# Kernel tuning notes

Hardware: AMD Instinct MI355X
Metric: run time of the kernel (lower is better)

The kernel has to match this reference:

```python
import jax, jax.numpy as jnp
import numpy as np

B, S, D, H, L, V = 2, 512, 1024, 16, 12, 50257
HD = D // H
DFF = 4 * D


def _ln(x, g, b, eps=1e-5):
    m = jnp.mean(x, axis=-1, keepdims=True)
    v = jnp.var(x, axis=-1, keepdims=True)
    return (x - m) * jax.lax.rsqrt(v + eps) * g + b


def setup_inputs() -> dict:
    key = jax.random.key(0)
    ks = jax.random.split(key, 32)
    sc = 0.02
    n = lambda k, shape: (jax.random.normal(k, shape, dtype=jnp.float32) * sc)
    inp = {
        "input_ids": jax.random.randint(ks[0], (B, S), 0, V, dtype=jnp.int64),
        "attention_mask": jnp.ones((B, S), dtype=jnp.float32),
        "image_hidden_states": jax.random.normal(ks[1], (B, D), dtype=jnp.float32),
        # token embedding table (also used for position embeds and tied lm_head, as in source)
        "wte": n(ks[2], (V, D)),
        # feature_space_transformation_nn: Linear(1024,1024) -> ReLU -> Linear(1024,1024)
        "ft_W1": n(ks[3], (D, D)), "ft_b1": jnp.zeros((D,), jnp.float32),
        "ft_W2": n(ks[4], (D, D)), "ft_b2": jnp.zeros((D,), jnp.float32),
        # per-layer params, stacked on leading L dim
        "ln1_g": jnp.ones((L, D), jnp.float32), "ln1_b": jnp.zeros((L, D), jnp.float32),
        "Wattn": n(ks[5], (L, D, 3 * D)), "battn": jnp.zeros((L, 3 * D), jnp.float32),
        "Wuk": n(ks[6], (L, D, D)), "buk": jnp.zeros((L, D), jnp.float32),
        "Wuv": n(ks[7], (L, D, D)), "buv": jnp.zeros((L, D), jnp.float32),
        "Wproj": n(ks[8], (L, D, D)), "bproj": jnp.zeros((L, D), jnp.float32),
        "ln2_g": jnp.ones((L, D), jnp.float32), "ln2_b": jnp.zeros((L, D), jnp.float32),
        "Wfc": n(ks[9], (L, D, DFF)), "bfc": jnp.zeros((L, DFF), jnp.float32),
        "Wfc2": n(ks[10], (L, DFF, D)), "bfc2": jnp.zeros((L, D), jnp.float32),
        "lnf_g": jnp.ones((D,), jnp.float32), "lnf_b": jnp.zeros((D,), jnp.float32),
    }
    return inp


def _forward(input_ids, attention_mask, image_hidden_states, wte,
             ft_W1, ft_b1, ft_W2, ft_b2,
             ln1_g, ln1_b, Wattn, battn, Wuk, buk, Wuv, buv, Wproj, bproj,
             ln2_g, ln2_b, Wfc, bfc, Wfc2, bfc2, lnf_g, lnf_b):
    # image feature transformation: Linear -> ReLU -> Linear
    img = jax.nn.relu(image_hidden_states @ ft_W1 + ft_b1) @ ft_W2 + ft_b2  # [B,D]

    # NOTE: source uses wte (not wpe) for position embeddings — faithful reproduction
    h = wte[input_ids] + wte[jnp.arange(S)][None]  # [B,S,D]

    # extended attention mask with a prepended zero column for the image token
    mask_ext = (1.0 - attention_mask)[:, None, None, :] * -10000.0  # [B,1,1,S]
    mask_ext = jnp.concatenate([jnp.zeros((B, 1, 1, 1), mask_ext.dtype), mask_ext], axis=-1)  # [B,1,1,S+1]

    # causal mask over kv_len=S+1: query i sees keys j <= i+1 (image token always visible)
    causal = jnp.arange(S + 1)[None, :] <= (jnp.arange(S)[:, None] + 1)  # [S,S+1]

    def block(h, p):
        (l1g, l1b, Wa, ba, Wk, bk, Wv, bv, Wp, bp, l2g, l2b, Wf, bf, Wf2, bf2) = p
        x = _ln(h, l1g, l1b)
        qkv = x @ Wa + ba
        q, k, v = jnp.split(qkv, 3, axis=-1)  # each [B,S,D]
        ki = (img @ Wk + bk)[:, None, :]  # [B,1,D]
        vi = (img @ Wv + bv)[:, None, :]
        k = jnp.concatenate([ki, k], axis=1)  # [B,S+1,D]
        v = jnp.concatenate([vi, v], axis=1)
        sh = lambda t, n: t.reshape(B, n, H, HD).transpose(0, 2, 1, 3)
        qh, kh, vh = sh(q, S), sh(k, S + 1), sh(v, S + 1)
        s = jnp.einsum('bhqd,bhkd->bhqk', qh, kh) / jnp.sqrt(jnp.float32(HD))
        s = jnp.where(causal[None, None], s, jnp.float32(-10000.0))
        s = s + mask_ext
        a = jax.nn.softmax(s, axis=-1)
        o = jnp.einsum('bhqk,bhkd->bhqd', a, vh).transpose(0, 2, 1, 3).reshape(B, S, D)
        h = h + (o @ Wp + bp)
        x = _ln(h, l2g, l2b)
        h = h + (jax.nn.gelu(x @ Wf + bf, approximate=True) @ Wf2 + bf2)
        return h, None

    params = (ln1_g, ln1_b, Wattn, battn, Wuk, buk, Wuv, buv, Wproj, bproj,
              ln2_g, ln2_b, Wfc, bfc, Wfc2, bfc2)
    h, _ = jax.lax.scan(block, h, params)
    h = _ln(h, lnf_g, lnf_b)
    return h @ wte.T  # tied lm head -> [B,S,V]


def reference(input_ids, attention_mask, image_hidden_states, wte,
              ft_W1, ft_b1, ft_W2, ft_b2,
              ln1_g, ln1_b, Wattn, battn, Wuk, buk, Wuv, buv, Wproj, bproj,
              ln2_g, ln2_b, Wfc, bfc, Wfc2, bfc2, lnf_g, lnf_b):
    return _forward(input_ids, attention_mask, image_hidden_states, wte,
                    ft_W1, ft_b1, ft_W2, ft_b2,
                    ln1_g, ln1_b, Wattn, battn, Wuk, buk, Wuv, buv, Wproj, bproj,
                    ln2_g, ln2_b, Wfc, bfc, Wfc2, bfc2, lnf_g, lnf_b)
```

## Files before the change

kernel.cpp:

```cpp
#include <hip/hip_runtime.h>
#include <cstdint>


typedef __bf16 bf16x8 __attribute__((ext_vector_type(8)));
typedef __bf16 bf16x4 __attribute__((ext_vector_type(4)));
typedef float  f32x4  __attribute__((ext_vector_type(4)));

#define GLDS16(g, l) __builtin_amdgcn_global_load_lds( \
    (const __attribute__((address_space(1))) unsigned int*)(g), \
    (__attribute__((address_space(3))) unsigned int*)(l), 16, 0, 0)

#define SCHED_FENCE() __builtin_amdgcn_sched_barrier(0)

__device__ __forceinline__ float gelu_f(float x) {
    float u = 1.5957691216057308f * (x + 0.044715f * x * x * x);
    float e = __expf(u);
    float t = 1.0f - 2.0f / (e + 1.0f);
    return 0.5f * x * (1.0f + t);
}

__device__ __forceinline__ int fragoff(int row, int kh, int hi) {
    return row * 64 + ((kh * 32 + hi * 8) ^ ((row & 7) << 3));
}
__device__ __forceinline__ int fragoff32(int row, int hi) {
    return row * 32 + ((hi ^ ((row >> 1) & 3)) << 3);
}

__device__ __forceinline__ void tcvt_body(
    int id, const float* __restrict__ Wa, const float* __restrict__ Wp,
    const float* __restrict__ Wf, const float* __restrict__ Wf2,
    __bf16* __restrict__ oa, __bf16* __restrict__ op,
    __bf16* __restrict__ of, __bf16* __restrict__ of2, float* tile)
{
    const float* src; __bf16* dst; int K, N, kb, nb;
    if (id < 768)       { src = Wa;  dst = oa;  K = 1024; N = 3072; kb = id & 15; nb = id >> 4; }
    else if (id < 1024) { id -= 768;  src = Wp;  dst = op;  K = 1024; N = 1024; kb = id & 15; nb = id >> 4; }
    else if (id < 2048) { id -= 1024; src = Wf;  dst = of;  K = 1024; N = 4096; kb = id & 15; nb = id >> 4; }
    else                { id -= 2048; src = Wf2; dst = of2; K = 4096; N = 1024; kb = id & 63; nb = id >> 6; }
    const int k0 = kb * 64, n0 = nb * 64;
    const int t = threadIdx.x;
    #pragma unroll
    for (int i = 0; i < 4; i++) {
        int r = i * 16 + (t >> 4), c = (t & 15) * 4;
        float4 v = *reinterpret_cast<const float4*>(src + (long)(k0 + r) * N + n0 + c);
        tile[r * 65 + c] = v.x; tile[r * 65 + c + 1] = v.y;
        tile[r * 65 + c + 2] = v.z; tile[r * 65 + c + 3] = v.w;
    }
    __syncthreads();
    const int nrow = t >> 2, kc = (t & 3) * 16;
    bf16x8 o0, o1;
    #pragma unroll
    for (int i = 0; i < 8; i++) {
        o0[i] = (__bf16)tile[(kc + i) * 65 + nrow];
        o1[i] = (__bf16)tile[(kc + 8 + i) * 65 + nrow];
    }
    *reinterpret_cast<bf16x8*>(dst + (long)(n0 + nrow) * K + k0 + kc)     = o0;
    *reinterpret_cast<bf16x8*>(dst + (long)(n0 + nrow) * K + k0 + kc + 8) = o1;
}

__device__ __forceinline__ void wcvt_body(
    int id, const float* __restrict__ wte, __bf16* __restrict__ out, long nvalid)
{
    long base = (long)id * 8192 + threadIdx.x * 8;
    #pragma unroll
    for (int i = 0; i < 4; i++) {
        long e = base + (long)i * 2048;
        bf16x8 o;
        if (e < nvalid) {
            float4 a = *reinterpret_cast<const float4*>(wte + e);
            float4 b = *reinterpret_cast<const float4*>(wte + e + 4);
            o[0] = (__bf16)a.x; o[1] = (__bf16)a.y; o[2] = (__bf16)a.z; o[3] = (__bf16)a.w;
            o[4] = (__bf16)b.x; o[5] = (__bf16)b.y; o[6] = (__bf16)b.z; o[7] = (__bf16)b.w;
        } else {
            #pragma unroll
            for (int q = 0; q < 8; q++) o[q] = (__bf16)0.f;
        }
        *reinterpret_cast<bf16x8*>(out + e) = o;
    }
}

__global__ __launch_bounds__(256) void tcvt_std(
    const float* __restrict__ Wa, const float* __restrict__ Wp,
    const float* __restrict__ Wf, const float* __restrict__ Wf2,
    __bf16* __restrict__ oa, __bf16* __restrict__ op,
    __bf16* __restrict__ of, __bf16* __restrict__ of2)
{
    __shared__ float tile[64 * 65];
    tcvt_body(blockIdx.x, Wa, Wp, Wf, Wf2, oa, op, of, of2, tile);
}

__global__ __launch_bounds__(256) void wcvt_std(
    const float* __restrict__ wte, __bf16* __restrict__ out, long nvalid)
{
    wcvt_body(blockIdx.x, wte, out, nvalid);
}

__global__ __launch_bounds__(256) void gemv_part(
    const float* __restrict__ x, int xld,
    const float* __restrict__ W, long wzs,
    float* __restrict__ part, int K, int N)
{
    int jb = blockIdx.x, kz = blockIdx.y, z = blockIdx.z;
    int t = threadIdx.x;
    int j = (jb << 6) + (t & 63);
    int g = t >> 6;
    int klen = K / (gridDim.y * 4);
    int kbase = (kz * 4 + g) * klen;
    const float* Wp = W + (long)z * wzs + (long)kbase * N + j;
    const float* x0 = x + kbase;
    const float* x1 = x + xld + kbase;
    float a0 = 0.f, a1 = 0.f;
    for (int k = 0; k < klen; k++) {
        float wv = Wp[(long)k * N];
        a0 += x0[k] * wv;
        a1 += x1[k] * wv;
    }
    __shared__ float r0[4][64], r1[4][64];
    r0[g][t & 63] = a0; r1[g][t & 63] = a1;
    __syncthreads();
    if (t < 64) {
        a0 = r0[0][t] + r0[1][t] + r0[2][t] + r0[3][t];
        a1 = r1[0][t] + r1[1][t] + r1[2][t] + r1[3][t];
        long base = (long)(z * gridDim.y + kz) * 2 * N + (jb << 6) + t;
        part[base]     = a0;
        part[base + N] = a1;
    }
}

__global__ __launch_bounds__(256) void gemv_reduce(
    const float* __restrict__ part, const float* __restrict__ bias, long bzs,
    float* __restrict__ out, int N, int nz, int act)
{
    int idx = blockIdx.x * 256 + threadIdx.x;
    if (idx >= nz * 2 * N) return;
    int j  = idx % N;
    int bz = idx / N;
    int z  = bz >> 1;
    float s = bias[(long)z * bzs + j];
    const float* p = part + ((long)z * 8 * 2 + (bz & 1)) * N + j;
    #pragma unroll
    for (int kz = 0; kz < 8; kz++) s += p[(long)kz * 2 * N];
    if (act) s = fmaxf(s, 0.f);
    out[idx] = s;
}

__global__ __launch_bounds__(256) void gemv_kv_part(
    const float* __restrict__ img,
    const float* __restrict__ Wuk, const float* __restrict__ Wuv,
    float* __restrict__ part)
{
    int jb = blockIdx.x, kz = blockIdx.y, z = blockIdx.z;
    int t = threadIdx.x;
    int j = (jb << 6) + (t & 63);
    int g = t >> 6;
    int kbase = (kz * 4 + g) * 64;
    const float* W = (z < 12) ? (Wuk + (long)z * 1048576) : (Wuv + (long)(z - 12) * 1048576);
    const float* Wp = W + (long)kbase * 1024 + j;
    const float* x0 = img + kbase;
    const float* x1 = img + 1024 + kbase;
    float a0 = 0.f, a1 = 0.f;
    for (int k = 0; k < 64; k++) {
        float wv = Wp[(long)k * 1024];
        a0 += x0[k] * wv;
        a1 += x1[k] * wv;
    }
    __shared__ float r0[4][64], r1[4][64];
    r0[g][t & 63] = a0; r1[g][t & 63] = a1;
    __syncthreads();
    if (t < 64) {
        a0 = r0[0][t] + r0[1][t] + r0[2][t] + r0[3][t];
        a1 = r1[0][t] + r1[1][t] + r1[2][t] + r1[3][t];
        long base = (long)(z * 4 + kz) * 2 * 1024 + (jb << 6) + t;
        part[base]        = a0;
        part[base + 1024] = a1;
    }
}

__global__ __launch_bounds__(256) void gemv_kv_reduce(
    const float* __restrict__ part,
    const float* __restrict__ buk, const float* __restrict__ buv,
    float* __restrict__ imgk, float* __restrict__ imgv)
{
    int idx = blockIdx.x * 256 + threadIdx.x;
    int z = idx >> 11;
    int bsel = (idx >> 10) & 1;
    int j = idx & 1023;
    float s = (z < 12) ? buk[z * 1024 + j] : buv[(z - 12) * 1024 + j];
    const float* p = part + ((long)z * 4 * 2 + bsel) * 1024 + j;
    #pragma unroll
    for (int kz = 0; kz < 4; kz++) s += p[(long)kz * 2 * 1024];
    if (z < 12) imgk[z * 2048 + bsel * 1024 + j] = s;
    else        imgv[(z - 12) * 2048 + bsel * 1024 + j] = s;
}

__global__ __launch_bounds__(256) void embed_ln(
    const int* __restrict__ ids, const float* __restrict__ wte,
    float* __restrict__ h, __bf16* __restrict__ xb,
    const float* __restrict__ g, const float* __restrict__ b)
{
    int row = blockIdx.x;
    int s = row & 511;
    int t = threadIdx.x;
    long id = ids[row];
    float4 v1 = reinterpret_cast<const float4*>(wte + id * 1024)[t];
    float4 v2 = reinterpret_cast<const float4*>(wte + (long)s * 1024)[t];
    float4 v; v.x = v1.x + v2.x; v.y = v1.y + v2.y; v.z = v1.z + v2.z; v.w = v1.w + v2.w;
    reinterpret_cast<float4*>(h + (long)row * 1024)[t] = v;

    float s1 = v.x + v.y + v.z + v.w;
    float s2 = v.x * v.x + v.y * v.y + v.z * v.z + v.w * v.w;
    #pragma unroll
    for (int o = 32; o >= 1; o >>= 1) { s1 += __shfl_xor(s1, o); s2 += __shfl_xor(s2, o); }
    __shared__ float r1[4], r2[4];
    int w = t >> 6;
    if ((t & 63) == 0) { r1[w] = s1; r2[w] = s2; }
    __syncthreads();
    s1 = r1[0] + r1[1] + r1[2] + r1[3];
    s2 = r2[0] + r2[1] + r2[2] + r2[3];
    float mean = s1 * (1.0f / 1024.0f);
    float var  = s2 * (1.0f / 1024.0f) - mean * mean;
    float rstd = rsqrtf(var + 1e-5f);
    float4 gg = reinterpret_cast<const float4*>(g)[t];
    float4 bb = reinterpret_cast<const float4*>(b)[t];
    bf16x4 o;
    o[0] = (__bf16)((v.x - mean) * rstd * gg.x + bb.x);
    o[1] = (__bf16)((v.y - mean) * rstd * gg.y + bb.y);
    o[2] = (__bf16)((v.z - mean) * rstd * gg.z + bb.z);
    o[3] = (__bf16)((v.w - mean) * rstd * gg.w + bb.w);
    *reinterpret_cast<bf16x4*>(xb + (long)row * 1024 + t * 4) = o;
}

__global__ __launch_bounds__(256) void ln_k(
    const float* __restrict__ in, __bf16* __restrict__ out,
    const float* __restrict__ g, const float* __restrict__ b)
{
    int row = blockIdx.x, t = threadIdx.x;
    float4 v = reinterpret_cast<const float4*>(in + (long)row * 1024)[t];
    float s1 = v.x + v.y + v.z + v.w;
    float s2 = v.x * v.x + v.y * v.y + v.z * v.z + v.w * v.w;
    #pragma unroll
    for (int o = 32; o >= 1; o >>= 1) { s1 += __shfl_xor(s1, o); s2 += __shfl_xor(s2, o); }
    __shared__ float r1[4], r2[4];
    int w = t >> 6;
    if ((t & 63) == 0) { r1[w] = s1; r2[w] = s2; }
    __syncthreads();
    s1 = r1[0] + r1[1] + r1[2] + r1[3];
    s2 = r2[0] + r2[1] + r2[2] + r2[3];
    float mean = s1 * (1.0f / 1024.0f);
    float var  = s2 * (1.0f / 1024.0f) - mean * mean;
    float rstd = rsqrtf(var + 1e-5f);
    float4 gg = reinterpret_cast<const float4*>(g)[t];
    float4 bb = reinterpret_cast<const float4*>(b)[t];
    bf16x4 o;
    o[0] = (__bf16)((v.x - mean) * rstd * gg.x + bb.x);
    o[1] = (__bf16)((v.y - mean) * rstd * gg.y + bb.y);
    o[2] = (__bf16)((v.z - mean) * rstd * gg.z + bb.z);
    o[3] = (__bf16)((v.w - mean) * rstd * gg.w + bb.w);
    *reinterpret_cast<bf16x4*>(out + (long)row * 1024 + t * 4) = o;
}

template<int NP>
__global__ __launch_bounds__(256) void lnadd_k(
    float* __restrict__ h, const float* __restrict__ part,
    const float* __restrict__ bias,
    const float* __restrict__ g, const float* __restrict__ b,
    __bf16* __restrict__ out)
{
    int row = blockIdx.x, t = threadIdx.x;
    long off = (long)row * 1024 + t * 4;
    float4 v = *reinterpret_cast<const float4*>(h + off);
    #pragma unroll
    for (int sp = 0; sp < NP; sp++) {
        float4 pv = *reinterpret_cast<const float4*>(part + sp * 1048576L + off);
        v.x += pv.x; v.y += pv.y; v.z += pv.z; v.w += pv.w;
    }
    float4 bi = reinterpret_cast<const float4*>(bias)[t];
    v.x += bi.x; v.y += bi.y; v.z += bi.z; v.w += bi.w;
    *reinterpret_cast<float4*>(h + off) = v;

    float s1 = v.x + v.y + v.z + v.w;
    float s2 = v.x * v.x + v.y * v.y + v.z * v.z + v.w * v.w;
    #pragma unroll
    for (int o = 32; o >= 1; o >>= 1) { s1 += __shfl_xor(s1, o); s2 += __shfl_xor(s2, o); }
    __shared__ float r1[4], r2[4];
    int w = t >> 6;
    if ((t & 63) == 0) { r1[w] = s1; r2[w] = s2; }
    __syncthreads();
    s1 = r1[0] + r1[1] + r1[2] + r1[3];
    s2 = r2[0] + r2[1] + r2[2] + r2[3];
    float mean = s1 * (1.0f / 1024.0f);
    float var  = s2 * (1.0f / 1024.0f) - mean * mean;
    float rstd = rsqrtf(var + 1e-5f);
    float4 gg = reinterpret_cast<const float4*>(g)[t];
    float4 bb = reinterpret_cast<const float4*>(b)[t];
    bf16x4 o;
    o[0] = (__bf16)((v.x - mean) * rstd * gg.x + bb.x);
    o[1] = (__bf16)((v.y - mean) * rstd * gg.y + bb.y);
    o[2] = (__bf16)((v.z - mean) * rstd * gg.z + bb.z);
    o[3] = (__bf16)((v.w - mean) * rstd * gg.w + bb.w);
    *reinterpret_cast<bf16x4*>(out + off) = o;
}

__global__ __launch_bounds__(512, 4) void gemm_lm2(
    const __bf16* __restrict__ A, const __bf16* __restrict__ Bt,
    float* __restrict__ C, int N, int K, int GM, int GN)
{
    const int total = GM * GN;
    const int q = total >> 3, r = total & 7;
    const int x = blockIdx.x & 7, jj = blockIdx.x >> 3;
    const int w0 = (x < r) ? x * (q + 1) + jj : r * (q + 1) + (x - r) * q + jj;
    const int m0 = (w0 % GM) * 128;
    const int n0 = (w0 / GM) * 256;

    __shared__ __bf16 As[3][128 * 32];
    __shared__ __bf16 Bs[3][256 * 32];
    const int t = threadIdx.x;
    const int wid = t >> 6, lane = t & 63;
    const int lo = lane & 15, hi = lane >> 4;
    const int wr = wid >> 2, wc = wid & 3;

    f32x4 acc[4][4] = {};

    const int srow = t >> 2;
    const int skx  = (((t & 3) ^ ((srow >> 1) & 3)) << 3);
    const int sldst = t * 8;
    #define STLM(bf, kk) do { \
        GLDS16(A + (long)(m0 + srow) * K + (kk) + skx, &As[bf][sldst]); \
        GLDS16(Bt + (long)(n0 + srow)       * K + (kk) + skx, &Bs[bf][sldst]); \
        GLDS16(Bt + (long)(n0 + 128 + srow) * K + (kk) + skx, &Bs[bf][4096 + sldst]); \
    } while (0)

    const int T = K >> 5;
    STLM(0, 0);
    if (T > 1) STLM(1, 32);
    int bcur = 0;
    for (int it = 0; it < T; it++) {
        if (it + 2 < T) {
            int bst = bcur >= 1 ? bcur - 1 : bcur + 2;
            STLM(bst, (it + 2) * 32);
            asm volatile("s_waitcnt vmcnt(6)" ::: "memory");
        } else if (it + 1 < T) {
            asm volatile("s_waitcnt vmcnt(3)" ::: "memory");
        } else {
            asm volatile("s_waitcnt vmcnt(0)" ::: "memory");
        }
        SCHED_FENCE();
        __builtin_amdgcn_s_barrier();
        SCHED_FENCE();

        bf16x8 afr[4], bfr[4];
        #pragma unroll
        for (int mi = 0; mi < 4; mi++)
            afr[mi] = *reinterpret_cast<const bf16x8*>(&As[bcur][fragoff32(wr * 64 + mi * 16 + lo, hi)]);
        #pragma unroll
        for (int ni = 0; ni < 4; ni++)
            bfr[ni] = *reinterpret_cast<const bf16x8*>(&Bs[bcur][fragoff32(wc * 64 + ni * 16 + lo, hi)]);
        __builtin_amdgcn_s_setprio(1);
        #pragma unroll
        for (int mi = 0; mi < 4; mi++)
            #pragma unroll
            for (int ni = 0; ni < 4; ni++)
                acc[mi][ni] = __builtin_amdgcn_mfma_f32_16x16x32_bf16(afr[mi], bfr[ni], acc[mi][ni], 0, 0, 0);
        __builtin_amdgcn_s_setprio(0);

        SCHED_FENCE();
        __builtin_amdgcn_s_barrier();
        SCHED_FENCE();
        bcur = bcur < 2 ? bcur + 1 : 0;
    }
    #undef STLM

    #pragma unroll
    for (int mi = 0; mi < 4; mi++)
        #pragma unroll
        for (int ni = 0; ni < 4; ni++) {
            int col = n0 + wc * 64 + ni * 16 + lo;
            if (col >= N) continue;
            #pragma unroll
            for (int rr = 0; rr < 4; rr++) {
                int row = m0 + wr * 64 + mi * 16 + hi * 4 + rr;
                C[(long)row * N + col] = acc[mi][ni][rr];
            }
        }
}

template<int BN, int OUTBF16, int ACT, int PARTIAL>
__global__ __launch_bounds__(256) void gemm64(
    const __bf16* __restrict__ A, const __bf16* __restrict__ Bt,
    const float* __restrict__ bias, void* __restrict__ C,
    int N, int K, int GM, int GN, int NS)
{
    constexpr int NB = BN / 32;
    constexpr int LP = 2 + NB;
    const int total = GM * GN * NS;
    const int q = total >> 3, r = total & 7;
    const int x = blockIdx.x & 7, jj = blockIdx.x >> 3;
    const int w0 = (x < r) ? x * (q + 1) + jj : r * (q + 1) + (x - r) * q + jj;
    const int sp = w0 / (GM * GN);
    const int rem = w0 - sp * (GM * GN);
    const int m0 = (rem % GM) * 64;
    const int n0 = (rem / GM) * BN;

    __shared__ __bf16 As[3][64 * 64];
    __shared__ __bf16 Bs[3][BN * 64];
    const int t = threadIdx.x;
    const int wv = t >> 6, lane = t & 63;
    const int lo = lane & 15, hi = lane >> 4;
    const int wr = wv >> 1, wc = wv & 1;

    f32x4 acc[2][NB] = {};

    const int srow = t >> 3;
    const int skx  = (((t & 7) ^ (srow & 7)) << 3);
    const int sldst = t * 8;
    #define ST64(bf, kk) do { \
        _Pragma("unroll") \
        for (int i = 0; i < 2; i++) \
            GLDS16(A + (long)(m0 + i * 32 + srow) * K + (kk) + skx, &As[bf][i * 2048 + sldst]); \
        _Pragma("unroll") \
        for (int i = 0; i < NB; i++) \
            GLDS16(Bt + (long)(n0 + i * 32 + srow) * K + (kk) + skx, &Bs[bf][i * 2048 + sldst]); \
    } while (0)

    const int Ksp = K / NS;
    const int kbeg = sp * Ksp;
    const int T = Ksp >> 6;

    ST64(0, kbeg);
    if (T > 1) ST64(1, kbeg + 64);
    int bcur = 0;
    for (int it = 0; it < T; it++) {
        if (it + 2 < T) {
            int bst = bcur >= 1 ? bcur - 1 : bcur + 2;
            ST64(bst, kbeg + (it + 2) * 64);
            asm volatile("s_waitcnt vmcnt(%0)" :: "i"(2 * LP) : "memory");
        } else if (it + 1 < T) {
            asm volatile("s_waitcnt vmcnt(%0)" :: "i"(LP) : "memory");
        } else {
            asm volatile("s_waitcnt vmcnt(0)" ::: "memory");
        }
        SCHED_FENCE();
        __builtin_amdgcn_s_barrier();
        SCHED_FENCE();

        #pragma unroll
        for (int kh = 0; kh < 2; kh++) {
            bf16x8 afr[2], bfr[NB];
            #pragma unroll
            for (int mi = 0; mi < 2; mi++)
                afr[mi] = *reinterpret_cast<const bf16x8*>(&As[bcur][fragoff(wr * 32 + mi * 16 + lo, kh, hi)]);
            #pragma unroll
            for (int ni = 0; ni < NB; ni++)
                bfr[ni] = *reinterpret_cast<const bf16x8*>(&Bs[bcur][fragoff(wc * (BN / 2) + ni * 16 + lo, kh, hi)]);
            __builtin_amdgcn_s_setprio(1);
            #pragma unroll
            for (int mi = 0; mi < 2; mi++)
                #pragma unroll
                for (int ni = 0; ni < NB; ni++)
                    acc[mi][ni] = __builtin_amdgcn_mfma_f32_16x16x32_bf16(afr[mi], bfr[ni], acc[mi][ni], 0, 0, 0);
            __builtin_amdgcn_s_setprio(0);
        }

        SCHED_FENCE();
        __builtin_amdgcn_s_barrier();
        SCHED_FENCE();
        bcur = bcur < 2 ? bcur + 1 : 0;
    }
    #undef ST64

    const long coff = PARTIAL ? (long)sp * GM * 64 * N : 0;
    #pragma unroll
    for (int mi = 0; mi < 2; mi++)
        #pragma unroll
        for (int ni = 0; ni < NB; ni++) {
            int col = n0 + wc * (BN / 2) + ni * 16 + lo;
            float bv = (!PARTIAL && bias) ? bias[col] : 0.f;
            #pragma unroll
            for (int rr = 0; rr < 4; rr++) {
                int row = m0 + wr * 32 + mi * 16 + hi * 4 + rr;
                float v = acc[mi][ni][rr] + bv;
                if (ACT) v = gelu_f(v);
                if (OUTBF16) ((__bf16*)C)[(long)row * N + col] = (__bf16)v;
                else         ((float*)C)[coff + (long)row * N + col] = v;
            }
        }
}

template<int OUTBF16, int ACT, int RES>
__global__ __launch_bounds__(256) void gemm_bb(
    const __bf16* __restrict__ A, const __bf16* __restrict__ Bt,
    const float* __restrict__ bias, const float* __restrict__ res,
    void* __restrict__ C, int N, int K)
{
    __shared__ __bf16 As[64 * 32];
    __shared__ __bf16 Bs[64 * 32];
    const int t = threadIdx.x;
    const int m0 = blockIdx.x * 64;
    const int n0 = blockIdx.y * 64;
    const int w = t >> 6, lane = t & 63;
    const int lo = lane & 15, hi = lane >> 4;
    const int wr = w >> 1, wc = w & 1;

    f32x4 acc[2][2] = {};

    for (int k0 = 0; k0 < K; k0 += 32) {
        __syncthreads();
        GLDS16(A  + (long)(m0 + (t >> 2)) * K + k0 + ((t & 3) << 3), &As[t * 8]);
        GLDS16(Bt + (long)(n0 + (t >> 2)) * K + k0 + ((t & 3) << 3), &Bs[t * 8]);
        __syncthreads();
        bf16x8 afr[2], bfr[2];
        #pragma unroll
        for (int mi = 0; mi < 2; mi++)
            afr[mi] = *reinterpret_cast<const bf16x8*>(&As[(wr * 32 + mi * 16 + lo) * 32 + hi * 8]);
        #pragma unroll
        for (int ni = 0; ni < 2; ni++)
            bfr[ni] = *reinterpret_cast<const bf16x8*>(&Bs[(wc * 32 + ni * 16 + lo) * 32 + hi * 8]);
        #pragma unroll
        for (int mi = 0; mi < 2; mi++)
            #pragma unroll
            for (int ni = 0; ni < 2; ni++)
                acc[mi][ni] = __builtin_amdgcn_mfma_f32_16x16x32_bf16(afr[mi], bfr[ni], acc[mi][ni], 0, 0, 0);
    }

    #pragma unroll
    for (int mi = 0; mi < 2; mi++)
        #pragma unroll
        for (int ni = 0; ni < 2; ni++) {
            int col = n0 + wc * 32 + ni * 16 + lo;
            float bv = bias ? bias[col] : 0.f;
            #pragma unroll
            for (int rr = 0; rr < 4; rr++) {
                int row = m0 + wr * 32 + mi * 16 + hi * 4 + rr;
                float v = acc[mi][ni][rr] + bv;
                if (ACT) v = gelu_f(v);
                if (RES) v += res[(long)row * N + col];
                if (OUTBF16) ((__bf16*)C)[(long)row * N + col] = (__bf16)v;
                else         ((float*)C)[(long)row * N + col] = v;
            }
        }
}

__global__ __launch_bounds__(256) void gemm_lm(
    const __bf16* __restrict__ A, const float* __restrict__ Wt,
    float* __restrict__ C, int N, int K)
{
    __shared__ __bf16 As[128 * 32];
    __shared__ __bf16 Bs[128 * 32];
    const int t = threadIdx.x;
    const int m0 = blockIdx.x * 128;
    const int n0 = blockIdx.y * 128;
    const int w = t >> 6, lane = t & 63;
    const int lo = lane & 15, hi = lane >> 4;
    const int wr = w >> 1, wc = w & 1;

    f32x4 acc[4][4] = {};

    for (int k0 = 0; k0 < K; k0 += 32) {
        __syncthreads();
        #pragma unroll
        for (int i = 0; i < 2; i++) {
            int c = i * 256 + t;
            GLDS16(A + (long)(m0 + (c >> 2)) * K + k0 + ((c & 3) << 3), &As[c * 8]);
        }
        #pragma unroll
        for (int i = 0; i < 2; i++) {
            int c = i * 256 + t;
            int nr = n0 + (c >> 2);
            bf16x8 bv;
            if (nr < N) {
                const float* wp = Wt + (long)nr * K + k0 + ((c & 3) << 3);
                float4 b0 = *reinterpret_cast<const float4*>(wp);
                float4 b1 = *reinterpret_cast<const float4*>(wp + 4);
                bv[0] = (__bf16)b0.x; bv[1] = (__bf16)b0.y; bv[2] = (__bf16)b0.z; bv[3] = (__bf16)b0.w;
                bv[4] = (__bf16)b1.x; bv[5] = (__bf16)b1.y; bv[6] = (__bf16)b1.z; bv[7] = (__bf16)b1.w;
            } else {
                #pragma unroll
                for (int qq = 0; qq < 8; qq++) bv[qq] = (__bf16)0.f;
            }
            *reinterpret_cast<bf16x8*>(&Bs[c * 8]) = bv;
        }
        __syncthreads();
        bf16x8 afr[4], bfr[4];
        #pragma unroll
        for (int mi = 0; mi < 4; mi++)
            afr[mi] = *reinterpret_cast<const bf16x8*>(&As[(wr * 64 + mi * 16 + lo) * 32 + hi * 8]);
        #pragma unroll
        for (int ni = 0; ni < 4; ni++)
            bfr[ni] = *reinterpret_cast<const bf16x8*>(&Bs[(wc * 64 + ni * 16 + lo) * 32 + hi * 8]);
        #pragma unroll
        for (int mi = 0; mi < 4; mi++)
            #pragma unroll
            for (int ni = 0; ni < 4; ni++)
                acc[mi][ni] = __builtin_amdgcn_mfma_f32_16x16x32_bf16(afr[mi], bfr[ni], acc[mi][ni], 0, 0, 0);
    }

    #pragma unroll
    for (int mi = 0; mi < 4; mi++)
        #pragma unroll
        for (int ni = 0; ni < 4; ni++) {
            int col = n0 + wc * 64 + ni * 16 + lo;
            if (col < N) {
                #pragma unroll
                for (int rr = 0; rr < 4; rr++) {
                    int row = m0 + wr * 64 + mi * 16 + hi * 4 + rr;
                    C[(long)row * N + col] = acc[mi][ni][rr];
                }
            }
        }
}

__global__ __launch_bounds__(256) void attn_aux(
    const __bf16* __restrict__ qkv,
    const float* __restrict__ imgk, const float* __restrict__ imgv,
    const float* __restrict__ amask, __bf16* __restrict__ out,
    int aux_mode,
    const float* __restrict__ Wa, const float* __restrict__ Wp,
    const float* __restrict__ Wf, const float* __restrict__ Wf2,
    __bf16* __restrict__ oa, __bf16* __restrict__ op,
    __bf16* __restrict__ of, __bf16* __restrict__ of2,
    const float* __restrict__ wte, __bf16* __restrict__ wteb, long nvalid)
{
    __shared__ __align__(16) char smem[28416];
    const int bid = blockIdx.x;
    if (bid >= 256) {
        if (aux_mode == 1)
            tcvt_body(bid - 256, Wa, Wp, Wf, Wf2, oa, op, of, of2, (float*)smem);
        else
            wcvt_body(bid - 256, wte, wteb, nvalid);
        return;
    }

    __bf16 (*Ks)[72] = (__bf16(*)[72])(smem);
    __bf16 (*Vt)[72] = (__bf16(*)[72])(smem + 9216);
    __bf16 (*Ps)[16][72] = (__bf16(*)[16][72])(smem + 18432);
    float* kimg_s = (float*)(smem + 27648);
    float* amv_s  = (float*)(smem + 27904);

    const int qb = bid & 7;
    const int h  = (bid >> 3) & 15;
    const int b  = bid >> 7;
    const int t = threadIdx.x, w = t >> 6, lane = t & 63;
    const int lo = lane & 15, hi = lane >> 4;

    const int kr8 = t >> 2, kd8 = (t & 3) * 16;
    const int vr8 = t & 63, vd8 = (t >> 6) * 16;

    const __bf16* qrow = qkv + (long)(b * 512 + qb * 64 + w * 16 + lo) * 3072 + h * 64;
    bf16x8 qf0 = *reinterpret_cast<const bf16x8*>(qrow + hi * 8);
    bf16x8 qf1 = *reinterpret_cast<const bf16x8*>(qrow + 32 + hi * 8);

    if (t < 64) kimg_s[t] = imgk[b * 1024 + h * 64 + t];
    __syncthreads();

    float simg = 0.f;
    #pragma unroll
    for (int i = 0; i < 8; i++)
        simg += (float)qf0[i] * kimg_s[hi * 8 + i] + (float)qf1[i] * kimg_s[32 + hi * 8 + i];
    simg += __shfl_xor(simg, 16);
    simg += __shfl_xor(simg, 32);
    simg *= 0.125f;

    float pimg[4], l_part[4];
    f32x4 o_acc[4];
    #pragma unroll
    for (int rr = 0; rr < 4; rr++) {
        pimg[rr] = __expf(__shfl(simg, hi * 4 + rr));
        l_part[rr] = 0.f;
    }
    #pragma unroll
    for (int df = 0; df < 4; df++) {
        float vi = imgv[b * 1024 + h * 64 + df * 16 + lo];
        #pragma unroll
        for (int rr = 0; rr < 4; rr++) o_acc[df][rr] = pimg[rr] * vi;
    }

    bf16x8 ck0, ck1, cv0, cv1;
    {
        const __bf16* ks = qkv + (long)(b * 512 + kr8) * 3072 + 1024 + h * 64 + kd8;
        ck0 = *reinterpret_cast<const bf16x8*>(ks);
        ck1 = *reinterpret_cast<const bf16x8*>(ks + 8);
        const __bf16* vs = qkv + (long)(b * 512 + vr8) * 3072 + 2048 + h * 64 + vd8;
        cv0 = *reinterpret_cast<const bf16x8*>(vs);
        cv1 = *reinterpret_cast<const bf16x8*>(vs + 8);
    }

    for (int kb = 0; kb <= qb; kb++) {
        bf16x8 nk0, nk1, nv0, nv1;
        const bool more = (kb < qb);
        if (more) {
            const __bf16* ks = qkv + (long)(b * 512 + (kb + 1) * 64 + kr8) * 3072 + 1024 + h * 64 + kd8;
            nk0 = *reinterpret_cast<const bf16x8*>(ks);
            nk1 = *reinterpret_cast<const bf16x8*>(ks + 8);
            const __bf16* vs = qkv + (long)(b * 512 + (kb + 1) * 64 + vr8) * 3072 + 2048 + h * 64 + vd8;
            nv0 = *reinterpret_cast<const bf16x8*>(vs);
            nv1 = *reinterpret_cast<const bf16x8*>(vs + 8);
        }
        __syncthreads();
        *reinterpret_cast<bf16x8*>(&Ks[kr8][kd8])     = ck0;
        *reinterpret_cast<bf16x8*>(&Ks[kr8][kd8 + 8]) = ck1;
        #pragma unroll
        for (int i = 0; i < 8; i++) { Vt[vd8 + i][vr8] = cv0[i]; Vt[vd8 + 8 + i][vr8] = cv1[i]; }
        if (t < 64) amv_s[t] = (1.0f - amask[b * 512 + kb * 64 + t]) * -10000.0f;
        __syncthreads();

        f32x4 sf[4];
        #pragma unroll
        for (int js = 0; js < 4; js++) {
            bf16x8 kf0 = *reinterpret_cast<const bf16x8*>(&Ks[js * 16 + lo][hi * 8]);
            bf16x8 kf1 = *reinterpret_cast<const bf16x8*>(&Ks[js * 16 + lo][32 + hi * 8]);
            f32x4 a = {};
            a = __builtin_amdgcn_mfma_f32_16x16x32_bf16(qf0, kf0, a, 0, 0, 0);
            a = __builtin_amdgcn_mfma_f32_16x16x32_bf16(qf1, kf1, a, 0, 0, 0);
            sf[js] = a;
        }
        #pragma unroll
        for (int js = 0; js < 4; js++) {
            float amv = amv_s[js * 16 + lo];
            #pragma unroll
            for (int rr = 0; rr < 4; rr++) {
                float sv = sf[js][rr] * 0.125f + amv;
                if (kb == qb) {
                    int qrw = w * 16 + hi * 4 + rr;
                    if (js * 16 + lo > qrw) sv = -10000.0f + amv;
                }
                float p = __expf(sv);
                l_part[rr] += p;
                Ps[w][hi * 4 + rr][js * 16 + lo] = (__bf16)p;
            }
        }
        #pragma unroll
        for (int jb = 0; jb < 2; jb++) {
            bf16x8 pf = *reinterpret_cast<const bf16x8*>(&Ps[w][lo][jb * 32 + hi * 8]);
            #pragma unroll
            for (int df = 0; df < 4; df++) {
                bf16x8 vf = *reinterpret_cast<const bf16x8*>(&Vt[df * 16 + lo][jb * 32 + hi * 8]);
                o_acc[df] = __builtin_amdgcn_mfma_f32_16x16x32_bf16(pf, vf, o_acc[df], 0, 0, 0);
            }
        }
        if (more) { ck0 = nk0; ck1 = nk1; cv0 = nv0; cv1 = nv1; }
    }

    float linv[4];
    #pragma unroll
    for (int rr = 0; rr < 4; rr++) {
        float ls = l_part[rr];
        #pragma unroll
        for (int off = 1; off < 16; off <<= 1) ls += __shfl_xor(ls, off);
        linv[rr] = 1.0f / (pimg[rr] + ls);
    }
    #pragma unroll
    for (int df = 0; df < 4; df++)
        #pragma unroll
        for (int rr = 0; rr < 4; rr++) {
            long row = b * 512 + qb * 64 + w * 16 + hi * 4 + rr;
            out[row * 1024 + h * 64 + df * 16 + lo] = (__bf16)(o_acc[df][rr] * linv[rr]);
        }
}

extern "C" void kernel_launch(void* const* d_in, const int* in_sizes, int n_in,
                              void* d_out, int out_size, void* d_ws, size_t ws_size,
                              hipStream_t stream) {
    (void)in_sizes; (void)n_in; (void)out_size;
    const int*   ids   = (const int*)d_in[0];
    const float* amask = (const float*)d_in[1];
    const float* ihs   = (const float*)d_in[2];
    const float* wte   = (const float*)d_in[3];
    const float* ftW1  = (const float*)d_in[4];
    const float* ftb1  = (const float*)d_in[5];
    const float* ftW2  = (const float*)d_in[6];
    const float* ftb2  = (const float*)d_in[7];
    const float* ln1g  = (const float*)d_in[8];
    const float* ln1b  = (const float*)d_in[9];
    const float* Wattn = (const float*)d_in[10];
    const float* battn = (const float*)d_in[11];
    const float* Wuk   = (const float*)d_in[12];
    const float* buk   = (const float*)d_in[13];
    const float* Wuv   = (const float*)d_in[14];
    const float* buv   = (const float*)d_in[15];
    const float* Wproj = (const float*)d_in[16];
    const float* bproj = (const float*)d_in[17];
    const float* ln2g  = (const float*)d_in[18];
    const float* ln2b  = (const float*)d_in[19];
    const float* Wfc   = (const float*)d_in[20];
    const float* bfc   = (const float*)d_in[21];
    const float* Wfc2  = (const float*)d_in[22];
    const float* bfc2  = (const float*)d_in[23];
    const float* lnfg  = (const float*)d_in[24];
    const float* lnfb  = (const float*)d_in[25];
    float* out = (float*)d_out;

    const long VP2 = 50432;
    const long NVALID = 50257L * 1024;
    char* base = (char*)d_ws;
    float* ftmp  = (float*)(base);
    float* img   = (float*)(base + (1 << 13));
    float* imgk  = (float*)(base + (1 << 14));
    float* imgv  = (float*)(base + 114688);
    float* part  = (float*)(base + 212992);
    float* h     = (float*)(base + 1048576);
    char* p = base + 5 * 1048576;
    __bf16* xb    = (__bf16*)p; p += 2 * 1048576;
    __bf16* qkvb  = (__bf16*)p; p += 6 * 1048576;
    __bf16* attob = (__bf16*)p; p += 2 * 1048576;
    __bf16* ffb   = (__bf16*)p; p += 8 * 1048576;
    __bf16* wtA0  = (__bf16*)p; p += 6 * 1048576;
    __bf16* wtP0  = (__bf16*)p; p += 2 * 1048576;
    __bf16* wtF0  = (__bf16*)p; p += 8 * 1048576;
    __bf16* wtF20 = (__bf16*)p; p += 8 * 1048576;
    __bf16* wteb  = (__bf16*)p; p += VP2 * 1024 * 2;
    size_t need1 = (size_t)(p - base);
    float* part_g = (float*)(base + need1);
    size_t need2 = need1 + 4 * 1048576 * sizeof(float);
    char* p2 = base + need2;
    __bf16* wtA1  = (__bf16*)p2; p2 += 6 * 1048576;
    __bf16* wtP1  = (__bf16*)p2; p2 += 2 * 1048576;
    __bf16* wtF1  = (__bf16*)p2; p2 += 8 * 1048576;
    __bf16* wtF21 = (__bf16*)p2; p2 += 8 * 1048576;
    size_t need3 = (size_t)(p2 - base);
    const bool big1 = (ws_size >= need1);
    const bool big2 = (ws_size >= need2);
    const bool big3 = (ws_size >= need3);

    __bf16* wtA_s[2]  = {wtA0, wtA1};
    __bf16* wtP_s[2]  = {wtP0, wtP1};
    __bf16* wtF_s[2]  = {wtF0, wtF1};
    __bf16* wtF2_s[2] = {wtF20, wtF21};

    dim3 b256(256);

    gemv_part<<<dim3(16, 8, 1), b256, 0, stream>>>(ihs, 1024, ftW1, 0, part, 1024, 1024);
    gemv_reduce<<<dim3(8), b256, 0, stream>>>(part, ftb1, 0, ftmp, 1024, 1, 1);
    gemv_part<<<dim3(16, 8, 1), b256, 0, stream>>>(ftmp, 1024, ftW2, 0, part, 1024, 1024);
    gemv_reduce<<<dim3(8), b256, 0, stream>>>(part, ftb2, 0, img, 1024, 1, 0);
    gemv_kv_part<<<dim3(16, 4, 24), b256, 0, stream>>>(img, Wuk, Wuv, part);
    gemv_kv_reduce<<<dim3(192), b256, 0, stream>>>(part, buk, buv, imgk, imgv);

    embed_ln<<<dim3(1024), b256, 0, stream>>>(ids, wte, h, xb, ln1g, ln1b);
    tcvt_std<<<dim3(3072), b256, 0, stream>>>(
        Wattn, Wproj, Wfc, Wfc2, wtA0, wtP0, wtF0, wtF20);

    for (int l = 0; l < 12; l++) {
        const int cs = big3 ? (l & 1) : 0;
        __bf16* cA  = wtA_s[cs];
        __bf16* cP  = wtP_s[cs];
        __bf16* cF  = wtF_s[cs];
        __bf16* cF2 = wtF2_s[cs];

        if (!big3 && l > 0) {
            tcvt_std<<<dim3(3072), b256, 0, stream>>>(
                Wattn + (long)l * 1024 * 3072, Wproj + (long)l * 1024 * 1024,
                Wfc + (long)l * 1024 * 4096, Wfc2 + (long)l * 4096 * 1024,
                wtA0, wtP0, wtF0, wtF20);
        }

        gemm64<128, 1, 0, 0><<<dim3(384), b256, 0, stream>>>(
            xb, cA, battn + l * 3072, qkvb, 3072, 1024, 16, 24, 1);

        if (big3 && l < 11) {
            const int ns = (l + 1) & 1;
            attn_aux<<<dim3(256 + 3072), b256, 0, stream>>>(
                qkvb, imgk + l * 2048, imgv + l * 2048, amask, attob, 1,
                Wattn + (long)(l + 1) * 1024 * 3072, Wproj + (long)(l + 1) * 1024 * 1024,
                Wfc + (long)(l + 1) * 1024 * 4096, Wfc2 + (long)(l + 1) * 4096 * 1024,
                wtA_s[ns], wtP_s[ns], wtF_s[ns], wtF2_s[ns],
                nullptr, nullptr, 0);
        } else if (big3 && l == 11) {
            attn_aux<<<dim3(256 + 6304), b256, 0, stream>>>(
                qkvb, imgk + l * 2048, imgv + l * 2048, amask, attob, 2,
                nullptr, nullptr, nullptr, nullptr,
                nullptr, nullptr, nullptr, nullptr,
                wte, wteb, NVALID);
        } else {
            attn_aux<<<dim3(256), b256, 0, stream>>>(
                qkvb, imgk + l * 2048, imgv + l * 2048, amask, attob, 0,
                nullptr, nullptr, nullptr, nullptr,
                nullptr, nullptr, nullptr, nullptr,
                nullptr, nullptr, 0);
        }

        const float* ng = (l < 11) ? (ln1g + (l + 1) * 1024) : lnfg;
        const float* nb = (l < 11) ? (ln1b + (l + 1) * 1024) : lnfb;
        if (big2) {
            gemm64<64, 0, 0, 1><<<dim3(512), b256, 0, stream>>>(
                attob, cP, nullptr, part_g, 1024, 1024, 16, 16, 2);
            lnadd_k<2><<<dim3(1024), b256, 0, stream>>>(
                h, part_g, bproj + l * 1024, ln2g + l * 1024, ln2b + l * 1024, xb);
            gemm64<128, 1, 1, 0><<<dim3(512), b256, 0, stream>>>(
                xb, cF, bfc + l * 4096, ffb, 4096, 1024, 16, 32, 1);
            gemm64<128, 0, 0, 1><<<dim3(512), b256, 0, stream>>>(
                ffb, cF2, nullptr, part_g, 1024, 4096, 16, 8, 4);
            lnadd_k<4><<<dim3(1024), b256, 0, stream>>>(
                h, part_g, bfc2 + l * 1024, ng, nb, xb);
        } else {
            gemm_bb<0, 0, 1><<<dim3(16, 16), b256, 0, stream>>>(
                attob, cP, bproj + l * 1024, h, h, 1024, 1024);
            ln_k<<<dim3(1024), b256, 0, stream>>>(h, xb, ln2g + l * 1024, ln2b + l * 1024);
            gemm64<128, 1, 1, 0><<<dim3(512), b256, 0, stream>>>(
                xb, cF, bfc + l * 4096, ffb, 4096, 1024, 16, 32, 1);
            gemm_bb<0, 0, 1><<<dim3(16, 16), b256, 0, stream>>>(
                ffb, cF2, bfc2 + l * 1024, h, h, 1024, 4096);
            ln_k<<<dim3(1024), b256, 0, stream>>>(h, xb, ng, nb);
        }
    }

    if (big1) {
        if (!big3)
            wcvt_std<<<dim3((unsigned)(VP2 * 1024 / 8192)), b256, 0, stream>>>(wte, wteb, NVALID);
        gemm_lm2<<<dim3(8 * (int)(VP2 / 256)), dim3(512), 0, stream>>>(
            xb, wteb, out, 50257, 1024, 8, (int)(VP2 / 256));
    } else {
        gemm_lm<<<dim3(8, 393), b256, 0, stream>>>(xb, wte, out, 50257, 1024);
    }
}
```

Before: 1.461 ms.

## Use 256x256 LM-head GEMM tiles with K=64 double-buffered phased staging

Replaces the 128x256 LM-head GEMM with a 256x256 tile kernel that stages K=64 slices into a 128KB double-buffered LDS region using an XOR swizzle. The next slice's loads are interleaved with the MFMA phases of the current slice. The grid is halved to 4 M-tiles per N-tile. The intent is to raise arithmetic intensity per loaded byte and hide global latency behind compute. The cost is lower occupancy (launch bounds 512,2), larger LDS use and more accumulator registers.

```diff
diff --git a/kernel.cpp b/kernel.cpp
--- a/kernel.cpp
+++ b/kernel.cpp
@@ -21,9 +21,6 @@
 
 __device__ __forceinline__ int fragoff(int row, int kh, int hi) {
     return row * 64 + ((kh * 32 + hi * 8) ^ ((row & 7) << 3));
-}
-__device__ __forceinline__ int fragoff32(int row, int hi) {
-    return row * 32 + ((hi ^ ((row >> 1) & 3)) << 3);
 }
 
 __device__ __forceinline__ void tcvt_body(
@@ -301,85 +298,121 @@
     *reinterpret_cast<bf16x4*>(out + off) = o;
 }
 
-__global__ __launch_bounds__(512, 4) void gemm_lm2(
+__shared__ __bf16 lm8_lds_dummy_decl_guard[1];
+
+__global__ __launch_bounds__(512, 2) void gemm_lm8(
     const __bf16* __restrict__ A, const __bf16* __restrict__ Bt,
     float* __restrict__ C, int N, int K, int GM, int GN)
 {
+    __shared__ __bf16 lds[65536];
     const int total = GM * GN;
     const int q = total >> 3, r = total & 7;
     const int x = blockIdx.x & 7, jj = blockIdx.x >> 3;
     const int w0 = (x < r) ? x * (q + 1) + jj : r * (q + 1) + (x - r) * q + jj;
-    const int m0 = (w0 % GM) * 128;
+    const int m0 = (w0 % GM) * 256;
     const int n0 = (w0 / GM) * 256;
 
-    __shared__ __bf16 As[3][128 * 32];
-    __shared__ __bf16 Bs[3][256 * 32];
     const int t = threadIdx.x;
     const int wid = t >> 6, lane = t & 63;
     const int lo = lane & 15, hi = lane >> 4;
     const int wr = wid >> 2, wc = wid & 3;
 
-    f32x4 acc[4][4] = {};
-
-    const int srow = t >> 2;
-    const int skx  = (((t & 3) ^ ((srow >> 1) & 3)) << 3);
-    const int sldst = t * 8;
-    #define STLM(bf, kk) do { \
-        GLDS16(A + (long)(m0 + srow) * K + (kk) + skx, &As[bf][sldst]); \
-        GLDS16(Bt + (long)(n0 + srow)       * K + (kk) + skx, &Bs[bf][sldst]); \
-        GLDS16(Bt + (long)(n0 + 128 + srow) * K + (kk) + skx, &Bs[bf][4096 + sldst]); \
-    } while (0)
-
-    const int T = K >> 5;
-    STLM(0, 0);
-    if (T > 1) STLM(1, 32);
-    int bcur = 0;
-    for (int it = 0; it < T; it++) {
-        if (it + 2 < T) {
-            int bst = bcur >= 1 ? bcur - 1 : bcur + 2;
-            STLM(bst, (it + 2) * 32);
-            asm volatile("s_waitcnt vmcnt(6)" ::: "memory");
-        } else if (it + 1 < T) {
-            asm volatile("s_waitcnt vmcnt(3)" ::: "memory");
+    f32x4 acc[8][4] = {};
+
+    const int srow = t >> 3;
+    const int skx  = (((t & 7) ^ (srow & 7)) << 3);
+    const int sdst = t * 8;
+
+#define A_OFF(db, hf) ((db) * 16384 + (hf) * 8192)
+#define B_OFF(db, hf) (32768 + (db) * 16384 + (hf) * 8192)
+#define STAGE_H(db, hsel, kt) do { \
+    const int h_ = (hsel) & 1; \
+    const __bf16* base_ = ((hsel) < 2) ? (A + (long)(m0 + h_ * 128) * K) \
+                                       : (Bt + (long)(n0 + h_ * 128) * K); \
+    const int d_ = ((hsel) < 2) ? A_OFF(db, h_) : B_OFF(db, h_); \
+    GLDS16(base_ + (long)srow * K + (kt) * 64 + skx,        &lds[d_ + sdst]); \
+    GLDS16(base_ + (long)(64 + srow) * K + (kt) * 64 + skx, &lds[d_ + 4096 + sdst]); \
+} while (0)
+
+#define PH(db, m, n, DOSTAGE) do { \
+    bf16x8 af_[4][2], bf_[2][2]; \
+    _Pragma("unroll") \
+    for (int mi = 0; mi < 4; mi++) \
+        _Pragma("unroll") \
+        for (int kh = 0; kh < 2; kh++) \
+            af_[mi][kh] = *reinterpret_cast<const bf16x8*>( \
+                &lds[A_OFF(db, wr) + fragoff(((m) * 4 + mi) * 16 + lo, kh, hi)]); \
+    _Pragma("unroll") \
+    for (int ni = 0; ni < 2; ni++) \
+        _Pragma("unroll") \
+        for (int kh = 0; kh < 2; kh++) \
+            bf_[ni][kh] = *reinterpret_cast<const bf16x8*>( \
+                &lds[B_OFF(db, wc >> 1) + fragoff((wc & 1) * 64 + ((n) * 2 + ni) * 16 + lo, kh, hi)]); \
+    DOSTAGE; \
+    asm volatile("s_waitcnt lgkmcnt(0)" ::: "memory"); \
+    SCHED_FENCE(); \
+    __builtin_amdgcn_s_setprio(1); \
+    _Pragma("unroll") \
+    for (int mi = 0; mi < 4; mi++) \
+        _Pragma("unroll") \
+        for (int ni = 0; ni < 2; ni++) \
+            _Pragma("unroll") \
+            for (int kh = 0; kh < 2; kh++) \
+                acc[(m) * 4 + mi][(n) * 2 + ni] = __builtin_amdgcn_mfma_f32_16x16x32_bf16( \
+                    af_[mi][kh], bf_[ni][kh], acc[(m) * 4 + mi][(n) * 2 + ni], 0, 0, 0); \
+    __builtin_amdgcn_s_setprio(0); \
+} while (0)
+
+    const int NKT = K >> 6;
+    STAGE_H(0, 0, 0); STAGE_H(0, 1, 0); STAGE_H(0, 2, 0); STAGE_H(0, 3, 0);
+
+    for (int i = 0; i < NKT / 2; i++) {
+        const int kt1 = 2 * i + 1, ktn = 2 * i + 2;
+        STAGE_H(1, 0, kt1);
+        asm volatile("s_waitcnt vmcnt(2)" ::: "memory");
+        SCHED_FENCE();
+        __builtin_amdgcn_s_barrier();
+        SCHED_FENCE();
+        PH(0, 0, 0, (void)0);
+        PH(0, 0, 1, STAGE_H(1, 1, kt1));
+        PH(0, 1, 0, STAGE_H(1, 2, kt1));
+        PH(0, 1, 1, STAGE_H(1, 3, kt1));
+        SCHED_FENCE();
+        __builtin_amdgcn_s_barrier();
+        SCHED_FENCE();
+        if (ktn < NKT) {
+            STAGE_H(0, 0, ktn);
+            asm volatile("s_waitcnt vmcnt(2)" ::: "memory");
         } else {
             asm volatile("s_waitcnt vmcnt(0)" ::: "memory");
         }
         SCHED_FENCE();
         __builtin_amdgcn_s_barrier();
         SCHED_FENCE();
-
-        bf16x8 afr[4], bfr[4];
-        #pragma unroll
-        for (int mi = 0; mi < 4; mi++)
-            afr[mi] = *reinterpret_cast<const bf16x8*>(&As[bcur][fragoff32(wr * 64 + mi * 16 + lo, hi)]);
-        #pragma unroll
-        for (int ni = 0; ni < 4; ni++)
-            bfr[ni] = *reinterpret_cast<const bf16x8*>(&Bs[bcur][fragoff32(wc * 64 + ni * 16 + lo, hi)]);
-        __builtin_amdgcn_s_setprio(1);
-        #pragma unroll
-        for (int mi = 0; mi < 4; mi++)
-            #pragma unroll
-            for (int ni = 0; ni < 4; ni++)
-                acc[mi][ni] = __builtin_amdgcn_mfma_f32_16x16x32_bf16(afr[mi], bfr[ni], acc[mi][ni], 0, 0, 0);
-        __builtin_amdgcn_s_setprio(0);
-
+        PH(1, 0, 0, (void)0);
+        PH(1, 0, 1, if (ktn < NKT) STAGE_H(0, 1, ktn));
+        PH(1, 1, 0, if (ktn < NKT) STAGE_H(0, 2, ktn));
+        PH(1, 1, 1, if (ktn < NKT) STAGE_H(0, 3, ktn));
         SCHED_FENCE();
         __builtin_amdgcn_s_barrier();
         SCHED_FENCE();
-        bcur = bcur < 2 ? bcur + 1 : 0;
-    }
-    #undef STLM
-
-    #pragma unroll
-    for (int mi = 0; mi < 4; mi++)
+    }
+#undef PH
+#undef STAGE_H
+#undef A_OFF
+#undef B_OFF
+
+    #pragma unroll
+    for (int mi = 0; mi < 8; mi++)
         #pragma unroll
         for (int ni = 0; ni < 4; ni++) {
             int col = n0 + wc * 64 + ni * 16 + lo;
-            if (col >= N) continue;
-            #pragma unroll
-            for (int rr = 0; rr < 4; rr++) {
-                int row = m0 + wr * 64 + mi * 16 + hi * 4 + rr;
-                C[(long)row * N + col] = acc[mi][ni][rr];
+            if (col < N) {
+                #pragma unroll
+                for (int rr = 0; rr < 4; rr++) {
+                    int row = m0 + wr * 128 + mi * 16 + hi * 4 + rr;
+                    C[(long)row * N + col] = acc[mi][ni][rr];
+                }
             }
         }
 }
@@ -906,8 +939,8 @@
     if (big1) {
         if (!big3)
             wcvt_std<<<dim3((unsigned)(VP2 * 1024 / 8192)), b256, 0, stream>>>(wte, wteb, NVALID);
-        gemm_lm2<<<dim3(8 * (int)(VP2 / 256)), dim3(512), 0, stream>>>(
-            xb, wteb, out, 50257, 1024, 8, (int)(VP2 / 256));
+        gemm_lm8<<<dim3(4 * (int)(VP2 / 256)), dim3(512), 0, stream>>>(
+            xb, wteb, out, 50257, 1024, 4, (int)(VP2 / 256));
     } else {
         gemm_lm<<<dim3(8, 393), b256, 0, stream>>>(xb, wte, out, 50257, 1024);
     }
```

Result: no change. 1.447 ms (-1.0%).
